# Kernel optimization log

Measured on AMD Instinct MI355X. Metric: run time of the kernel, lower is better.

## Reference

```python
import jax, jax.numpy as jnp
import numpy as np

EPS = 1e-12  # matches torch F.normalize eps default

def _l2_normalize(x, axis=-1):
    n = jnp.linalg.norm(x, axis=axis, keepdims=True)
    return x / jnp.maximum(n, EPS)

def setup_inputs() -> dict:
    key = jax.random.key(0)
    k1, k2, k3 = jax.random.split(key, 3)
    B, N, D = 1024, 500000, 128
    return {
        "query_embeddings": jax.random.normal(k1, (B, D), dtype=jnp.float32),
        "memory_keys": jax.random.normal(k2, (N, D), dtype=jnp.float32),
        "memory_values": jax.random.normal(k3, (N, D), dtype=jnp.float32),
        "top_k": 8,
    }

def reference(query_embeddings, memory_keys, memory_values, top_k):
    # L2-normalize queries and memory keys (torch F.normalize, p=2)
    q = _l2_normalize(query_embeddings, axis=1)        # [B, D]
    k = _l2_normalize(memory_keys, axis=1)             # [N, D]
    # Cosine similarities: [B, N]
    sims = jnp.einsum('bd,nd->bn', q, k)
    # Top-k (largest, sorted) per query
    _, topk_idx = jax.lax.top_k(sims, top_k)           # [B, k]
    # Gather values: [B, k, D]
    retrieved = memory_values[topk_idx]
    return retrieved
```

## Files before the change

kernel.cpp:

```cpp
#include <hip/hip_runtime.h>


#define DIM 128
#define TOPK 8
#define THR0 0.30f
#define CHUNKS 128
#define QPB 256
#define NCAND 24

typedef _Float16 half8 __attribute__((ext_vector_type(8)));
typedef _Float16 half2v __attribute__((ext_vector_type(2)));
typedef float f32x4 __attribute__((ext_vector_type(4)));

__global__ __launch_bounds__(256) void norm_rows_kernel(const float* __restrict__ in,
                                                        _Float16* __restrict__ outh,
                                                        int rows) {
  int row = blockIdx.x * 4 + (threadIdx.x >> 6);
  int lane = threadIdx.x & 63;
  if (row >= rows) return;
  float2 v = *(const float2*)(in + (size_t)row * DIM + lane * 2);
  float ss = v.x * v.x + v.y * v.y;
#pragma unroll
  for (int off = 32; off; off >>= 1) ss += __shfl_xor(ss, off);
  float inv = 1.0f / fmaxf(sqrtf(ss), 1e-12f);
  half2v o;
  o.x = (_Float16)(v.x * inv);
  o.y = (_Float16)(v.y * inv);
  *(half2v*)(outh + (size_t)row * DIM + lane * 2) = o;
}

__global__ __launch_bounds__(1024) void score_select_kernel(
    const _Float16* __restrict__ qh, const _Float16* __restrict__ kh,
    float* __restrict__ cscore, int* __restrict__ cidx, int N, int iters) {
  __shared__ _Float16 ktile[2][64 * 136];
  __shared__ float lscore[QPB * 8];
  __shared__ int lidx[QPB * 8];
  __shared__ float thrL[QPB];

  const int tid = threadIdx.x;
  const int lane = tid & 63;
  const int w = tid >> 6;
  const int col = lane & 15;
  const int quad = lane >> 4;
  const int qg = blockIdx.x;
  const int chunk = blockIdx.y;
  const long chunk_base = (long)chunk * iters * 64;

  for (int e = tid; e < QPB * 8; e += 1024) {
    lscore[e] = -1e30f;
    lidx[e] = 0;
  }
  if (tid < QPB) thrL[tid] = THR0;

  half8 bf[4];
  {
    const _Float16* qrow = qh + ((size_t)qg * QPB + w * 16 + col) * DIM + quad * 8;
#pragma unroll
    for (int t = 0; t < 4; t++) bf[t] = *(const half8*)(qrow + t * 32);
  }

  const int srow = tid >> 4;
  const int scol = tid & 15;
  const int ld_off = srow * 136 + scol * 8;

  float4 staged;
  {
    long key = chunk_base + srow;
    if (key < (long)N)
      staged = *(const float4*)(kh + key * (size_t)DIM + scol * 8);
    else
      staged.x = staged.y = staged.z = staged.w = 0.f;
  }

  float thr_cur = THR0;
  for (int it = 0; it < iters; ++it) {
    *(float4*)(ktile[it & 1] + ld_off) = staged;
    __syncthreads();
    if (it + 1 < iters) {
      long key = chunk_base + (long)(it + 1) * 64 + srow;
      if (key < (long)N)
        staged = *(const float4*)(kh + key * (size_t)DIM + scol * 8);
      else
        staged.x = staged.y = staged.z = staged.w = 0.f;
    }
    const _Float16* kt = ktile[it & 1];
    const long keyb_it = chunk_base + (long)it * 64;
#pragma unroll
    for (int sub = 0; sub < 4; ++sub) {
      const _Float16* arow = kt + (sub * 16 + col) * 136 + quad * 8;
      f32x4 acc = {0.f, 0.f, 0.f, 0.f};
#pragma unroll
      for (int t = 0; t < 4; t++) {
        half8 af = *(const half8*)(arow + t * 32);
        acc = __builtin_amdgcn_mfma_f32_16x16x32_f16(af, bf[t], acc, 0, 0, 0);
      }
      float mx = fmaxf(fmaxf(acc[0], acc[1]), fmaxf(acc[2], acc[3]));
      if (__any(mx > thr_cur)) {
        const long keyb = keyb_it + sub * 16;
#pragma unroll
        for (int r = 0; r < 4; ++r) {
          float av = acc[r];
          unsigned long long m = __ballot(av > thr_cur);
          while (m) {
            int src = __ffsll(m) - 1;
            m &= m - 1;
            float sc = __shfl(av, src);
            int qq = w * 16 + (src & 15);
            long kk = keyb + (src >> 4) * 4 + r;
            if (lane == 0 && kk < (long)N) {
              float* Ls = lscore + qq * 8;
              int* Li = lidx + qq * 8;
              float mn = Ls[0];
              int ms = 0;
#pragma unroll
              for (int s2 = 1; s2 < 8; s2++) {
                float vv = Ls[s2];
                if (vv < mn) { mn = vv; ms = s2; }
              }
              if (sc > mn) {
                Ls[ms] = sc;
                Li[ms] = (int)kk;
                float nm = Ls[0];
#pragma unroll
                for (int s2 = 1; s2 < 8; s2++) nm = fminf(nm, Ls[s2]);
                thrL[qq] = fmaxf(THR0, nm);
              }
            }
          }
        }
        thr_cur = thrL[w * 16 + col];
      }
    }
  }
  __syncthreads();
  for (int e = tid; e < QPB * 8; e += 1024) {
    int ql = e >> 3, slot = e & 7;
    size_t o = ((size_t)qg * QPB + ql) * (CHUNKS * 8) + (size_t)chunk * 8 + slot;
    cscore[o] = lscore[e];
    cidx[o] = lidx[e];
  }
}

__global__ __launch_bounds__(64) void merge_rescore_kernel(
    const float* __restrict__ Q, const float* __restrict__ Kf, const float* __restrict__ V,
    const float* __restrict__ cscore, const int* __restrict__ cidx,
    float* __restrict__ out, int N) {
  const int q = blockIdx.x;
  const int lane = threadIdx.x;
  const int E = CHUNKS * 8;
  float s[16];
  int ii[16];
#pragma unroll
  for (int i = 0; i < 16; i++) {
    size_t o = (size_t)q * E + i * 64 + lane;
    s[i] = cscore[o];
    ii[i] = cidx[o];
  }
  __shared__ int topI[NCAND];
  __shared__ double simsL[NCAND];
  unsigned consumed = 0;
  for (int t = 0; t < NCAND; t++) {
    float bv = -3e38f;
    int bid = 0x7fffffff;
    int bpos = -1;
#pragma unroll
    for (int i = 0; i < 16; i++) {
      float v = ((consumed >> i) & 1) ? -3e38f : s[i];
      if (v > bv || (v == bv && ii[i] < bid)) { bv = v; bid = ii[i]; bpos = i; }
    }
    float myv = bv;
    int myi = bid;
#pragma unroll
    for (int off = 32; off; off >>= 1) {
      float ov = __shfl_xor(bv, off);
      int oi = __shfl_xor(bid, off);
      if (ov > bv || (ov == bv && oi < bid)) { bv = ov; bid = oi; }
    }
    if (bv <= -1e29f) {
      if (lane == 0)
        for (int z = t; z < NCAND; z++) topI[z] = -1;
      break;
    }
    if (bpos >= 0 && myv == bv && myi == bid) consumed |= 1u << bpos;
    if (lane == 0) topI[t] = bid;
  }
  __syncthreads();

  float q0 = Q[(size_t)q * DIM + lane];
  float q1 = Q[(size_t)q * DIM + 64 + lane];
  double dq = (double)q0 * q0 + (double)q1 * q1;
#pragma unroll
  for (int off = 32; off; off >>= 1) dq += __shfl_xor(dq, off);
  double qn = fmax(sqrt(dq), 1e-12);
  for (int c = 0; c < NCAND; ++c) {
    int id = topI[c];
    int idc = id < 0 ? 0 : id;
    float kx = Kf[(size_t)idc * DIM + lane];
    float ky = Kf[(size_t)idc * DIM + 64 + lane];
    double dot = (double)q0 * kx + (double)q1 * ky;
    double ks = (double)kx * kx + (double)ky * ky;
#pragma unroll
    for (int off = 32; off; off >>= 1) {
      dot += __shfl_xor(dot, off);
      ks += __shfl_xor(ks, off);
    }
    double sim = dot / (qn * fmax(sqrt(ks), 1e-12));
    if (lane == 0) simsL[c] = (id >= 0) ? sim : -1e300;
  }
  __syncthreads();

  unsigned used = 0;
  for (int j = 0; j < TOPK; j++) {
    double bv = -1e301;
    int bc = -1;
    int bid = 0x7fffffff;
    for (int c = 0; c < NCAND; c++) {
      if ((used >> c) & 1) continue;
      int id = topI[c];
      if (id < 0) continue;
      double v = simsL[c];
      if (v > bv || (v == bv && id < bid)) { bv = v; bid = id; bc = c; }
    }
    int row = 0;
    if (bc >= 0) {
      used |= 1u << bc;
      row = topI[bc];
    }
    out[((size_t)q * TOPK + j) * DIM + lane] = V[(size_t)row * DIM + lane];
    out[((size_t)q * TOPK + j) * DIM + 64 + lane] = V[(size_t)row * DIM + 64 + lane];
  }
}

extern "C" void kernel_launch(void* const* d_in, const int* in_sizes, int n_in,
                              void* d_out, int out_size, void* d_ws, size_t ws_size,
                              hipStream_t stream) {
  const float* Q = (const float*)d_in[0];
  const float* Kf = (const float*)d_in[1];
  const float* V = (const float*)d_in[2];
  float* out = (float*)d_out;
  const int B = in_sizes[0] / DIM;
  const int N = in_sizes[1] / DIM;

  char* ws = (char*)d_ws;
  size_t cand_elems = (size_t)B * CHUNKS * 8;
  float* cscore = (float*)ws;
  int* cidx = (int*)(ws + cand_elems * 4);
  _Float16* qh = (_Float16*)(ws + cand_elems * 8);
  _Float16* kh = (_Float16*)(ws + cand_elems * 8 + (size_t)B * DIM * 2);

  int iters = (N + CHUNKS * 64 - 1) / (CHUNKS * 64);

  norm_rows_kernel<<<dim3((B + 3) / 4), 256, 0, stream>>>(Q, qh, B);
  norm_rows_kernel<<<dim3((N + 3) / 4), 256, 0, stream>>>(Kf, kh, N);
  score_select_kernel<<<dim3(B / QPB, CHUNKS), 1024, 0, stream>>>(qh, kh, cscore, cidx, N, iters);
  merge_rescore_kernel<<<dim3(B), 64, 0, stream>>>(Q, Kf, V, cscore, cidx, out, N);
}
```

Baseline: 698.4 us.

## Split waves into query/key sets with dual accumulators and merge per-set top lists

Measured after the change: 688.7 us. About the same (-1.4%).

```diff
diff --git a/kernel.cpp b/kernel.cpp
--- a/kernel.cpp
+++ b/kernel.cpp
@@ -9,54 +9,61 @@
 #define NCAND 24
 
 typedef _Float16 half8 __attribute__((ext_vector_type(8)));
-typedef _Float16 half2v __attribute__((ext_vector_type(2)));
+typedef _Float16 half4v __attribute__((ext_vector_type(4)));
 typedef float f32x4 __attribute__((ext_vector_type(4)));
 
 __global__ __launch_bounds__(256) void norm_rows_kernel(const float* __restrict__ in,
                                                         _Float16* __restrict__ outh,
                                                         int rows) {
-  int row = blockIdx.x * 4 + (threadIdx.x >> 6);
-  int lane = threadIdx.x & 63;
+  int row = blockIdx.x * 8 + (threadIdx.x >> 5);
+  int l = threadIdx.x & 31;
   if (row >= rows) return;
-  float2 v = *(const float2*)(in + (size_t)row * DIM + lane * 2);
-  float ss = v.x * v.x + v.y * v.y;
-#pragma unroll
-  for (int off = 32; off; off >>= 1) ss += __shfl_xor(ss, off);
+  float4 v = *(const float4*)(in + (size_t)row * DIM + l * 4);
+  float ss = v.x * v.x + v.y * v.y + v.z * v.z + v.w * v.w;
+#pragma unroll
+  for (int off = 16; off; off >>= 1) ss += __shfl_xor(ss, off);
   float inv = 1.0f / fmaxf(sqrtf(ss), 1e-12f);
-  half2v o;
+  half4v o;
   o.x = (_Float16)(v.x * inv);
   o.y = (_Float16)(v.y * inv);
-  *(half2v*)(outh + (size_t)row * DIM + lane * 2) = o;
+  o.z = (_Float16)(v.z * inv);
+  o.w = (_Float16)(v.w * inv);
+  *(half4v*)(outh + (size_t)row * DIM + l * 4) = o;
 }
 
 __global__ __launch_bounds__(1024) void score_select_kernel(
     const _Float16* __restrict__ qh, const _Float16* __restrict__ kh,
     float* __restrict__ cscore, int* __restrict__ cidx, int N, int iters) {
   __shared__ _Float16 ktile[2][64 * 136];
-  __shared__ float lscore[QPB * 8];
-  __shared__ int lidx[QPB * 8];
-  __shared__ float thrL[QPB];
+  __shared__ float lscore[2][QPB * 8];
+  __shared__ int lidx[2][QPB * 8];
+  __shared__ float thrL[2][QPB];
 
   const int tid = threadIdx.x;
   const int lane = tid & 63;
   const int w = tid >> 6;
   const int col = lane & 15;
   const int quad = lane >> 4;
+  const int qset = w & 7;
+  const int kset = w >> 3;
   const int qg = blockIdx.x;
   const int chunk = blockIdx.y;
   const long chunk_base = (long)chunk * iters * 64;
 
-  for (int e = tid; e < QPB * 8; e += 1024) {
-    lscore[e] = -1e30f;
-    lidx[e] = 0;
-  }
-  if (tid < QPB) thrL[tid] = THR0;
-
-  half8 bf[4];
+  for (int e = tid; e < 2 * QPB * 8; e += 1024) {
+    ((float*)lscore)[e] = -1e30f;
+    ((int*)lidx)[e] = 0;
+  }
+  if (tid < 2 * QPB) ((float*)thrL)[tid] = THR0;
+
+  half8 bf[2][4];
   {
-    const _Float16* qrow = qh + ((size_t)qg * QPB + w * 16 + col) * DIM + quad * 8;
-#pragma unroll
-    for (int t = 0; t < 4; t++) bf[t] = *(const half8*)(qrow + t * 32);
+    const _Float16* qrow = qh + ((size_t)qg * QPB + qset * 32 + col) * DIM + quad * 8;
+#pragma unroll
+    for (int t = 0; t < 4; t++) {
+      bf[0][t] = *(const half8*)(qrow + t * 32);
+      bf[1][t] = *(const half8*)(qrow + 16 * DIM + t * 32);
+    }
   }
 
   const int srow = tid >> 4;
@@ -72,7 +79,7 @@
       staged.x = staged.y = staged.z = staged.w = 0.f;
   }
 
-  float thr_cur = THR0;
+  float thr0 = THR0, thr1 = THR0;
   for (int it = 0; it < iters; ++it) {
     *(float4*)(ktile[it & 1] + ld_off) = staged;
     __syncthreads();
@@ -86,58 +93,88 @@
     const _Float16* kt = ktile[it & 1];
     const long keyb_it = chunk_base + (long)it * 64;
 #pragma unroll
-    for (int sub = 0; sub < 4; ++sub) {
+    for (int ss = 0; ss < 2; ++ss) {
+      const int sub = kset * 2 + ss;
       const _Float16* arow = kt + (sub * 16 + col) * 136 + quad * 8;
-      f32x4 acc = {0.f, 0.f, 0.f, 0.f};
+      f32x4 acc0 = {0.f, 0.f, 0.f, 0.f};
+      f32x4 acc1 = {0.f, 0.f, 0.f, 0.f};
 #pragma unroll
       for (int t = 0; t < 4; t++) {
         half8 af = *(const half8*)(arow + t * 32);
-        acc = __builtin_amdgcn_mfma_f32_16x16x32_f16(af, bf[t], acc, 0, 0, 0);
+        acc0 = __builtin_amdgcn_mfma_f32_16x16x32_f16(af, bf[0][t], acc0, 0, 0, 0);
+        acc1 = __builtin_amdgcn_mfma_f32_16x16x32_f16(af, bf[1][t], acc1, 0, 0, 0);
       }
-      float mx = fmaxf(fmaxf(acc[0], acc[1]), fmaxf(acc[2], acc[3]));
-      if (__any(mx > thr_cur)) {
+      float mx0 = fmaxf(fmaxf(acc0[0], acc0[1]), fmaxf(acc0[2], acc0[3]));
+      float mx1 = fmaxf(fmaxf(acc1[0], acc1[1]), fmaxf(acc1[2], acc1[3]));
+      if (__any(mx0 > thr0 || mx1 > thr1)) {
         const long keyb = keyb_it + sub * 16;
 #pragma unroll
-        for (int r = 0; r < 4; ++r) {
-          float av = acc[r];
-          unsigned long long m = __ballot(av > thr_cur);
-          while (m) {
-            int src = __ffsll(m) - 1;
-            m &= m - 1;
-            float sc = __shfl(av, src);
-            int qq = w * 16 + (src & 15);
-            long kk = keyb + (src >> 4) * 4 + r;
-            if (lane == 0 && kk < (long)N) {
-              float* Ls = lscore + qq * 8;
-              int* Li = lidx + qq * 8;
-              float mn = Ls[0];
-              int ms = 0;
-#pragma unroll
-              for (int s2 = 1; s2 < 8; s2++) {
-                float vv = Ls[s2];
-                if (vv < mn) { mn = vv; ms = s2; }
-              }
-              if (sc > mn) {
-                Ls[ms] = sc;
-                Li[ms] = (int)kk;
-                float nm = Ls[0];
-#pragma unroll
-                for (int s2 = 1; s2 < 8; s2++) nm = fminf(nm, Ls[s2]);
-                thrL[qq] = fmaxf(THR0, nm);
+        for (int h = 0; h < 2; ++h) {
+          const float thrH = h ? thr1 : thr0;
+#pragma unroll
+          for (int r = 0; r < 4; ++r) {
+            float av = h ? acc1[r] : acc0[r];
+            unsigned long long m = __ballot(av > thrH);
+            while (m) {
+              int src = __ffsll(m) - 1;
+              m &= m - 1;
+              float sc = __shfl(av, src);
+              int qq = qset * 32 + h * 16 + (src & 15);
+              long kk = keyb + (src >> 4) * 4 + r;
+              if (lane == 0 && kk < (long)N) {
+                float* Ls = lscore[kset] + qq * 8;
+                int* Li = lidx[kset] + qq * 8;
+                float mn = Ls[0];
+                int ms = 0;
+#pragma unroll
+                for (int s2 = 1; s2 < 8; s2++) {
+                  float vv = Ls[s2];
+                  if (vv < mn) { mn = vv; ms = s2; }
+                }
+                if (sc > mn) {
+                  Ls[ms] = sc;
+                  Li[ms] = (int)kk;
+                  float nm = Ls[0];
+#pragma unroll
+                  for (int s2 = 1; s2 < 8; s2++) nm = fminf(nm, Ls[s2]);
+                  thrL[kset][qq] = fmaxf(THR0, nm);
+                }
               }
             }
           }
         }
-        thr_cur = thrL[w * 16 + col];
+        thr0 = thrL[kset][qset * 32 + col];
+        thr1 = thrL[kset][qset * 32 + 16 + col];
       }
     }
   }
   __syncthreads();
-  for (int e = tid; e < QPB * 8; e += 1024) {
-    int ql = e >> 3, slot = e & 7;
-    size_t o = ((size_t)qg * QPB + ql) * (CHUNKS * 8) + (size_t)chunk * 8 + slot;
-    cscore[o] = lscore[e];
-    cidx[o] = lidx[e];
+  if (tid < QPB) {
+    const int ql = tid;
+    float s16[16];
+    int i16[16];
+#pragma unroll
+    for (int j = 0; j < 8; j++) {
+      s16[j] = lscore[0][ql * 8 + j];
+      i16[j] = lidx[0][ql * 8 + j];
+      s16[8 + j] = lscore[1][ql * 8 + j];
+      i16[8 + j] = lidx[1][ql * 8 + j];
+    }
+    size_t base = ((size_t)qg * QPB + ql) * (CHUNKS * 8) + (size_t)chunk * 8;
+    unsigned used = 0;
+#pragma unroll
+    for (int sl = 0; sl < 8; sl++) {
+      float bv = -3e38f;
+      int bp = 0;
+#pragma unroll
+      for (int j = 0; j < 16; j++) {
+        float v = ((used >> j) & 1) ? -3e38f : s16[j];
+        if (v > bv) { bv = v; bp = j; }
+      }
+      used |= 1u << bp;
+      cscore[base + sl] = s16[bp];
+      cidx[base + sl] = i16[bp];
+    }
   }
 }
 
@@ -250,8 +287,8 @@
 
   int iters = (N + CHUNKS * 64 - 1) / (CHUNKS * 64);
 
-  norm_rows_kernel<<<dim3((B + 3) / 4), 256, 0, stream>>>(Q, qh, B);
-  norm_rows_kernel<<<dim3((N + 3) / 4), 256, 0, stream>>>(Kf, kh, N);
+  norm_rows_kernel<<<dim3((B + 7) / 8), 256, 0, stream>>>(Q, qh, B);
+  norm_rows_kernel<<<dim3((N + 7) / 8), 256, 0, stream>>>(Kf, kh, N);
   score_select_kernel<<<dim3(B / QPB, CHUNKS), 1024, 0, stream>>>(qh, kh, cscore, cidx, N, iters);
   merge_rescore_kernel<<<dim3(B), 64, 0, stream>>>(Q, Kf, V, cscore, cidx, out, N);
 }
```
